# Optimization experiments

Measured on AMD Instinct MI355X. Metric: run time of the kernel, lower is better.

## Reference

```python
import jax, jax.numpy as jnp
import numpy as np

NUM_HEADS = 4
CATEGORY_SIZE = 128
DIM = 192
B, N, M = 2, 65000, 64


def setup_inputs() -> dict:
    key = jax.random.key(0)
    k1, k2, k3, k4 = jax.random.split(key, 4)
    qkv = jax.random.normal(k1, (B, N, 3 * DIM), dtype=jnp.float32)
    sim = jax.random.normal(k2, (B, N, M), dtype=jnp.float32)
    proj_w = jax.random.normal(k3, (DIM, DIM), dtype=jnp.float32) * (1.0 / np.sqrt(DIM))
    proj_b = jax.random.normal(k4, (DIM,), dtype=jnp.float32) * 0.01
    logit_scale = jnp.log(10.0 * jnp.ones((1, 1), dtype=jnp.float32))
    return {"qkv": qkv, "sim": sim, "proj_w": proj_w, "proj_b": proj_b,
            "logit_scale": logit_scale, "x_size": 65000}


def reference(qkv, sim, proj_w, proj_b, logit_scale, x_size):
    b, n, c3 = qkv.shape
    c = c3 // 3
    h = NUM_HEADS
    gs = min(n, CATEGORY_SIZE)
    ng = (n + gs - 1) // gs
    pad_n = ng * gs - n

    # token -> category id, then sort tokens by category
    tk_id = jnp.argmax(sim, axis=-1)                      # (b, n) int
    sort_idx = jnp.argsort(tk_id, axis=-1)                # (b, n)
    inv_idx = jnp.argsort(sort_idx, axis=-1)              # inverse permutation

    shuffled = jnp.take_along_axis(qkv, sort_idx[..., None], axis=1)  # (b, n, 3c)
    if pad_n > 0:
        pad = jnp.flip(shuffled[:, n - pad_n:n, :], axis=1)
        shuffled = jnp.concatenate([shuffled, pad], axis=1)           # (b, n+pad_n, 3c)

    # (3, b, ng, h, gs, c/h)
    y = shuffled.reshape(b, ng, gs, 3, h, c // h).transpose(3, 0, 1, 4, 2, 5)
    q, k, v = y[0], y[1], y[2]

    scale = jnp.exp(jnp.minimum(logit_scale, jnp.log(jnp.asarray(100.0, dtype=qkv.dtype))))
    attn = jnp.einsum('bghqd,bghkd->bghqk', q, k) * scale  # (b, ng, h, gs, gs)
    attn = jax.nn.softmax(attn, axis=-1)
    out = jnp.einsum('bghqk,bghkd->bghqd', attn, v)        # (b, ng, h, gs, c/h)
    out = out.transpose(0, 1, 3, 2, 4).reshape(b, n + pad_n, c)[:, :n, :]

    # scatter back to original token order
    out = jnp.take_along_axis(out, inv_idx[..., None], axis=1)
    return out @ proj_w.T + proj_b
```

## Files before the change

### kernel.cpp

```cpp
#include <hip/hip_runtime.h>
#include <hip/hip_bf16.h>
#include <math.h>

#define BB 2
#define NN 65000
#define MM 64
#define DIM 192
#define NH 4
#define HD 48
#define GS 128
#define NG 508
#define SORT_TPB 256
#define NBLK 254

#define XROWS 65024
#define XTILES_B 1016

typedef __attribute__((ext_vector_type(8))) short bf16x8;
typedef __attribute__((ext_vector_type(8))) _Float16 f16x8;
typedef __attribute__((ext_vector_type(2))) __fp16 fp16x2;
typedef __attribute__((ext_vector_type(4))) float f32x4;
typedef __attribute__((ext_vector_type(16))) float f32x16;
typedef __attribute__((ext_vector_type(8))) unsigned short u16x8;

__device__ __forceinline__ unsigned short f2bf(float f) {
  __hip_bfloat16 h = __float2bfloat16(f);
  return *(unsigned short*)&h;
}
__device__ __forceinline__ unsigned int pkh(float lo, float hi) {
  fp16x2 t = __builtin_amdgcn_cvt_pkrtz(lo, hi);
  return *(unsigned int*)&t;
}
__device__ __forceinline__ f16x8 cvt8h(float4 a, float4 b) {
  f16x8 r;
  r[0] = (_Float16)a.x; r[1] = (_Float16)a.y; r[2] = (_Float16)a.z; r[3] = (_Float16)a.w;
  r[4] = (_Float16)b.x; r[5] = (_Float16)b.y; r[6] = (_Float16)b.z; r[7] = (_Float16)b.w;
  return r;
}
__device__ __forceinline__ void gload_lds16(const float* src, float* lds_dst) {
  __builtin_amdgcn_global_load_lds(
      (const __attribute__((address_space(1))) unsigned int*)src,
      (__attribute__((address_space(3))) unsigned int*)lds_dst, 16, 0, 0);
}

__global__ void k_argmax_hist(const float* __restrict__ sim, int* __restrict__ tk,
                              int* __restrict__ hist) {
  __shared__ int cnt[MM];
  const int b = blockIdx.y, blk = blockIdx.x;
  if (threadIdx.x < MM) cnt[threadIdx.x] = 0;
  __syncthreads();
  int t = blk * SORT_TPB + threadIdx.x;
  if (t < NN) {
    const float4* row = (const float4*)(sim + ((size_t)b * NN + t) * MM);
    float best = -INFINITY;
    int bi = 0;
#pragma unroll
    for (int j = 0; j < MM / 4; ++j) {
      float4 v = row[j];
      if (v.x > best) { best = v.x; bi = 4 * j + 0; }
      if (v.y > best) { best = v.y; bi = 4 * j + 1; }
      if (v.z > best) { best = v.z; bi = 4 * j + 2; }
      if (v.w > best) { best = v.w; bi = 4 * j + 3; }
    }
    tk[b * NN + t] = bi;
    atomicAdd(&cnt[bi], 1);
  }
  __syncthreads();
  if (threadIdx.x < MM)
    hist[(b * NBLK + blk) * MM + threadIdx.x] = cnt[threadIdx.x];
}

#define SEGS 16
#define SEGB 16
__global__ void k_scan(const int* __restrict__ hist, int* __restrict__ boff) {
  const int b = blockIdx.x;
  const int tid = threadIdx.x;
  const int seg = tid >> 6, bin = tid & 63;
  __shared__ int part[SEGS][MM];
  __shared__ int basev[MM];
  const int lo = seg * SEGB;
  const int hi = min(NBLK, lo + SEGB);
  int s = 0;
  for (int blk = lo; blk < hi; ++blk) s += hist[(b * NBLK + blk) * MM + bin];
  part[seg][bin] = s;
  __syncthreads();
  if (tid < 64) {
    int tot = 0;
#pragma unroll
    for (int s2 = 0; s2 < SEGS; ++s2) tot += part[s2][bin];
    int incl = tot;
#pragma unroll
    for (int d = 1; d < 64; d <<= 1) {
      int o = __shfl_up(incl, d);
      if (bin >= d) incl += o;
    }
    basev[bin] = incl - tot;
  }
  __syncthreads();
  int run = basev[bin];
  for (int s2 = 0; s2 < seg; ++s2) run += part[s2][bin];
  for (int blk = lo; blk < hi; ++blk) {
    int h = hist[(b * NBLK + blk) * MM + bin];
    boff[(b * NBLK + blk) * MM + bin] = run;
    run += h;
  }
}

__global__ void k_scatter(const int* __restrict__ tk, const int* __restrict__ boff,
                          int* __restrict__ sidx) {
  __shared__ int whist[4][MM];
  const int b = blockIdx.y, blk = blockIdx.x;
  const int tid = threadIdx.x;
  const int w = tid >> 6, lane = tid & 63;
  ((int*)whist)[tid] = 0;
  __syncthreads();
  int t = blk * SORT_TPB + tid;
  int bin = (t < NN) ? tk[b * NN + t] : -1;
  unsigned long long m = ~0ull;
#pragma unroll
  for (int bit = 0; bit < 6; ++bit) {
    unsigned long long bl = __ballot((bin >> bit) & 1);
    m &= ((bin >> bit) & 1) ? bl : ~bl;
  }
  int rank_w = __popcll(m & ((1ull << lane) - 1ull));
  if (bin >= 0 && rank_w == 0) whist[w][bin] = __popcll(m);
  __syncthreads();
  if (bin >= 0) {
    int rank = rank_w;
#pragma unroll
    for (int w2 = 0; w2 < 3; ++w2)
      if (w2 < w) rank += whist[w2][bin];
    int pos = boff[(b * NBLK + blk) * MM + bin] + rank;
    sidx[b * NN + pos] = t;
  }
}

__global__ __launch_bounds__(256) void k_attn_mfma(const float* __restrict__ qkv,
                                                   const int* __restrict__ sidx,
                                                   const float* __restrict__ logit_scale,
                                                   __hip_bfloat16* __restrict__ attn_out) {
  const int x = blockIdx.x;
  const int g = ((x >> 4) << 3) + (x & 7);
  const int p = (x >> 3) & 1;
  const int b = blockIdx.z;
  if (g >= NG) return;
  const int hd0 = 2 * p;

  __shared__ int stok[GS];
  __shared__ __align__(16) _Float16 akv2[2][4 * 3 * 64 * 8];
  __shared__ __align__(16) _Float16 vfrag2[2][2 * 8 * 64 * 8];

  const int tid = threadIdx.x;
  const int w = tid >> 6, l = tid & 63;
  const int hl = l >> 5, l31 = l & 31;

  if (tid < GS) {
    int s = g * GS + tid;
    int sp = (s < NN) ? s : (2 * NN - 1 - s);
    stok[tid] = sidx[b * NN + sp];
  }
  __syncthreads();

#pragma unroll
  for (int head = 0; head < 2; ++head)
#pragma unroll
    for (int i = 0; i < 3; ++i) {
      int cc = tid + 256 * i;
      int ts = cc >> 6, cl = cc & 63;
      int kvr = (ts / 3) * 32 + (cl & 31);
      int dbase = (ts % 3) * 16 + (cl >> 5) * 8;
      const float* src = qkv + (size_t)(b * NN + stok[kvr]) * (3 * DIM) + DIM + (hd0 + head) * HD + dbase;
      ((f16x8*)akv2[head])[cc] = cvt8h(((const float4*)src)[0], ((const float4*)src)[1]);
    }

#pragma unroll
  for (int head = 0; head < 2; ++head)
#pragma unroll
    for (int i = 0; i < 4; ++i) {
      int cc = tid + 256 * i;
      int ntks = cc >> 6, cl = cc & 63;
      int nt = ntks >> 3, ks = ntks & 7;
      int d = nt * 32 + (cl & 31);
      int kvb = ks * 16 + (cl >> 5) * 8;
      _Float16 tmp[8];
      if (d < HD) {
#pragma unroll
        for (int e = 0; e < 8; ++e)
          tmp[e] = (_Float16)qkv[(size_t)(b * NN + stok[kvb + e]) * (3 * DIM) + 2 * DIM + (hd0 + head) * HD + d];
      } else {
#pragma unroll
        for (int e = 0; e < 8; ++e) tmp[e] = (_Float16)0.f;
      }
      ((f16x8*)vfrag2[head])[cc] = *(f16x8*)tmp;
    }

  f16x8 qf[2][3];
  {
    const float* qb = qkv + (size_t)(b * NN + stok[w * 32 + l31]) * (3 * DIM);
#pragma unroll
    for (int head = 0; head < 2; ++head)
#pragma unroll
      for (int s = 0; s < 3; ++s) {
        const float4* ptr = (const float4*)(qb + (hd0 + head) * HD + s * 16 + hl * 8);
        qf[head][s] = cvt8h(ptr[0], ptr[1]);
      }
  }
  __syncthreads();

  const float scale = expf(fminf(logit_scale[0], 4.6051701860f));

  for (int hh = 0; hh < 2; ++hh) {
    const int hd = hd0 + hh;

    f32x16 accS[4];
#pragma unroll
    for (int t = 0; t < 4; ++t)
#pragma unroll
      for (int r = 0; r < 16; ++r) accS[t][r] = 0.f;

#pragma unroll
    for (int t = 0; t < 4; ++t)
#pragma unroll
      for (int s = 0; s < 3; ++s) {
        f16x8 af = ((const f16x8*)akv2[hh])[(t * 3 + s) * 64 + l];
        accS[t] = __builtin_amdgcn_mfma_f32_32x32x16_f16(af, qf[hh][s], accS[t], 0, 0, 0);
      }

    float mx = -INFINITY;
#pragma unroll
    for (int t = 0; t < 4; ++t)
#pragma unroll
      for (int r = 0; r < 16; ++r) { accS[t][r] *= scale; mx = fmaxf(mx, accS[t][r]); }
    mx = fmaxf(mx, __shfl_xor(mx, 32));
    float sum = 0.f;
#pragma unroll
    for (int t = 0; t < 4; ++t)
#pragma unroll
      for (int r = 0; r < 16; ++r) { float pv = __expf(accS[t][r] - mx); accS[t][r] = pv; sum += pv; }
    sum += __shfl_xor(sum, 32);
    const float inv = 1.f / sum;
#pragma unroll
    for (int t = 0; t < 4; ++t)
#pragma unroll
      for (int r = 0; r < 16; ++r) accS[t][r] *= inv;

    f32x16 accO[2];
#pragma unroll
    for (int nt = 0; nt < 2; ++nt)
#pragma unroll
      for (int r = 0; r < 16; ++r) accO[nt][r] = 0.f;

#pragma unroll
    for (int t = 0; t < 4; ++t) {
      union { unsigned int u[4]; f16x8 v; } fa, fb;
      {
        unsigned int a0 = pkh(accS[t][0], accS[t][1]);
        unsigned int a1 = pkh(accS[t][2], accS[t][3]);
        unsigned int b0 = pkh(accS[t][4], accS[t][5]);
        unsigned int b1 = pkh(accS[t][6], accS[t][7]);
        unsigned int sa0 = __shfl_xor(a0, 32), sa1 = __shfl_xor(a1, 32);
        unsigned int sb0 = __shfl_xor(b0, 32), sb1 = __shfl_xor(b1, 32);
        fa.u[0] = hl ? sb0 : a0; fa.u[1] = hl ? sb1 : a1;
        fa.u[2] = hl ? b0 : sa0; fa.u[3] = hl ? b1 : sa1;
      }
      {
        unsigned int a0 = pkh(accS[t][8], accS[t][9]);
        unsigned int a1 = pkh(accS[t][10], accS[t][11]);
        unsigned int b0 = pkh(accS[t][12], accS[t][13]);
        unsigned int b1 = pkh(accS[t][14], accS[t][15]);
        unsigned int sa0 = __shfl_xor(a0, 32), sa1 = __shfl_xor(a1, 32);
        unsigned int sb0 = __shfl_xor(b0, 32), sb1 = __shfl_xor(b1, 32);
        fb.u[0] = hl ? sb0 : a0; fb.u[1] = hl ? sb1 : a1;
        fb.u[2] = hl ? b0 : sa0; fb.u[3] = hl ? b1 : sa1;
      }
      accO[0] = __builtin_amdgcn_mfma_f32_32x32x16_f16(fa.v, ((const f16x8*)vfrag2[hh])[(0 * 8 + 2 * t) * 64 + l], accO[0], 0, 0, 0);
      accO[1] = __builtin_amdgcn_mfma_f32_32x32x16_f16(fa.v, ((const f16x8*)vfrag2[hh])[(1 * 8 + 2 * t) * 64 + l], accO[1], 0, 0, 0);
      accO[0] = __builtin_amdgcn_mfma_f32_32x32x16_f16(fb.v, ((const f16x8*)vfrag2[hh])[(0 * 8 + 2 * t + 1) * 64 + l], accO[0], 0, 0, 0);
      accO[1] = __builtin_amdgcn_mfma_f32_32x32x16_f16(fb.v, ((const f16x8*)vfrag2[hh])[(1 * 8 + 2 * t + 1) * 64 + l], accO[1], 0, 0, 0);
    }

#pragma unroll
    for (int r = 0; r < 16; ++r) {
      int rowl = w * 32 + (r & 3) + 8 * (r >> 2) + 4 * hl;
      int sg = g * GS + rowl;
      if (sg < NN) {
        size_t base = ((size_t)b * XROWS + sg) * DIM + hd * HD;
        attn_out[base + l31] = __float2bfloat16(accO[0][r]);
        if (l31 < 16) attn_out[base + 32 + l31] = __float2bfloat16(accO[1][r]);
      }
    }
  }
}

__global__ void k_wpack(const float* __restrict__ W, unsigned short* __restrict__ wpack) {
  int idx = blockIdx.x * blockDim.x + threadIdx.x;
  if (idx >= 12 * 6 * 64) return;
  int lane = idx & 63;
  int kkjt = idx >> 6;
  int kk = kkjt % 6;
  int jt = kkjt / 6;
  int j = jt * 16 + (lane & 15);
  int k0 = kk * 32 + (lane >> 4) * 8;
  const float* src = W + (size_t)j * DIM + k0;
  unsigned short tmp[8];
#pragma unroll
  for (int e = 0; e < 8; ++e) tmp[e] = f2bf(src[e]);
  ((u16x8*)wpack)[idx] = *(const u16x8*)tmp;
}

__global__ __launch_bounds__(256) void k_proj_mfma(const unsigned short* __restrict__ xb,
                                                   const int* __restrict__ sidx,
                                                   const unsigned short* __restrict__ wpack,
                                                   const float* __restrict__ bias,
                                                   float* __restrict__ out) {
  __shared__ unsigned short wl[12 * 6 * 64 * 8];
  const int tid = threadIdx.x;

#pragma unroll
  for (int j = 0; j < 18; ++j) {
    int c = j * 256 + tid;
    gload_lds16((const float*)((const u16x8*)wpack + c), (float*)((u16x8*)wl + c));
  }

  const int wid = tid >> 6, lane = tid & 63;
  const int l15 = lane & 15, lk = lane >> 4;

  float bv[12];
#pragma unroll
  for (int jt = 0; jt < 12; ++jt) bv[jt] = bias[jt * 16 + l15];

  __syncthreads();

  for (int tile = blockIdx.x; tile < BB * XTILES_B; tile += gridDim.x) {
    const int b = tile / XTILES_B;
    const int r0 = (tile % XTILES_B) * 64 + wid * 16;
    f32x4 acc[12];
#pragma unroll
    for (int jt = 0; jt < 12; ++jt) { f32x4 t = {bv[jt], bv[jt], bv[jt], bv[jt]}; acc[jt] = t; }

    const unsigned short* xrow = xb + ((size_t)b * XROWS + r0 + l15) * DIM;
#pragma unroll
    for (int kk = 0; kk < 6; ++kk) {
      bf16x8 a = *(const bf16x8*)(xrow + kk * 32 + lk * 8);
#pragma unroll
      for (int jt = 0; jt < 12; ++jt) {
        bf16x8 bfr = *(const bf16x8*)(wl + ((jt * 6 + kk) * 64 + lane) * 8);
        acc[jt] = __builtin_amdgcn_mfma_f32_16x16x32_bf16(a, bfr, acc[jt], 0, 0, 0);
      }
    }

    const int rowb = r0 + lk * 4;
    int orow[4];
#pragma unroll
    for (int r = 0; r < 4; ++r)
      orow[r] = (rowb + r < NN) ? sidx[b * NN + rowb + r] : -1;

#pragma unroll
    for (int jt = 0; jt < 12; ++jt) {
#pragma unroll
      for (int r = 0; r < 4; ++r) {
        if (orow[r] >= 0)
          out[((size_t)b * NN + orow[r]) * DIM + jt * 16 + l15] = acc[jt][r];
      }
    }
  }
}

extern "C" void kernel_launch(void* const* d_in, const int* in_sizes, int n_in,
                              void* d_out, int out_size, void* d_ws, size_t ws_size,
                              hipStream_t stream) {
  const float* qkv = (const float*)d_in[0];
  const float* sim = (const float*)d_in[1];
  const float* proj_w = (const float*)d_in[2];
  const float* proj_b = (const float*)d_in[3];
  const float* logit_scale = (const float*)d_in[4];

  unsigned short* x_bf16 = (unsigned short*)d_ws;
  unsigned short* wpack = x_bf16 + (size_t)BB * XROWS * DIM;
  int* tk = (int*)(wpack + 12 * 6 * 64 * 8);
  int* hist = tk + (size_t)BB * NN;
  int* boff = hist + (size_t)BB * NBLK * MM;
  int* sidx = boff + (size_t)BB * NBLK * MM;

  k_argmax_hist<<<dim3(NBLK, BB), SORT_TPB, 0, stream>>>(sim, tk, hist);
  k_scan<<<BB, 1024, 0, stream>>>(hist, boff);
  k_scatter<<<dim3(NBLK, BB), SORT_TPB, 0, stream>>>(tk, boff, sidx);
  k_wpack<<<(12 * 6 * 64 + 255) / 256, 256, 0, stream>>>(proj_w, wpack);
  k_attn_mfma<<<dim3(1024, 1, BB), 256, 0, stream>>>(qkv, sidx, logit_scale,
                                                     (__hip_bfloat16*)x_bf16);
  k_proj_mfma<<<dim3(1016), 256, 0, stream>>>(x_bf16, sidx, wpack, proj_b, (float*)d_out);
}
```

Before: 171.0 us.

## Load K/V rows coalesced into padded LDS and gather MFMA fragments from LDS

Replaces the strided global gathers that built pre-swizzled K and V fragment buffers with coalesced float4 row loads of K and V into padded row-major LDS tiles (stride 100 halves). K fragments are then read from LDS as two 4-wide loads, and V fragments are built with scalar 16-bit LDS reads per element. The aim is to cut the scattered per-element global V loads; the cost is many more LDS instructions in the PV loop and possible bank conflicts. Launch bounds also now request 3 blocks per CU.

```diff
diff --git a/kernel.cpp b/kernel.cpp
--- a/kernel.cpp
+++ b/kernel.cpp
@@ -16,8 +16,11 @@
 #define XROWS 65024
 #define XTILES_B 1016
 
+#define KVS 100
+
 typedef __attribute__((ext_vector_type(8))) short bf16x8;
 typedef __attribute__((ext_vector_type(8))) _Float16 f16x8;
+typedef __attribute__((ext_vector_type(4))) _Float16 f16x4;
 typedef __attribute__((ext_vector_type(2))) __fp16 fp16x2;
 typedef __attribute__((ext_vector_type(4))) float f32x4;
 typedef __attribute__((ext_vector_type(16))) float f32x16;
@@ -135,20 +138,19 @@
   }
 }
 
-__global__ __launch_bounds__(256) void k_attn_mfma(const float* __restrict__ qkv,
-                                                   const int* __restrict__ sidx,
-                                                   const float* __restrict__ logit_scale,
-                                                   __hip_bfloat16* __restrict__ attn_out) {
+__global__ __launch_bounds__(256, 3) void k_attn_mfma(const float* __restrict__ qkv,
+                                                      const int* __restrict__ sidx,
+                                                      const float* __restrict__ logit_scale,
+                                                      __hip_bfloat16* __restrict__ attn_out) {
   const int x = blockIdx.x;
   const int g = ((x >> 4) << 3) + (x & 7);
   const int p = (x >> 3) & 1;
   const int b = blockIdx.z;
   if (g >= NG) return;
-  const int hd0 = 2 * p;
 
   __shared__ int stok[GS];
-  __shared__ __align__(16) _Float16 akv2[2][4 * 3 * 64 * 8];
-  __shared__ __align__(16) _Float16 vfrag2[2][2 * 8 * 64 * 8];
+  __shared__ __align__(16) _Float16 kls[GS * KVS];
+  __shared__ __align__(16) _Float16 vls[GS * KVS];
 
   const int tid = threadIdx.x;
   const int w = tid >> 6, l = tid & 63;
@@ -162,47 +164,28 @@
   __syncthreads();
 
 #pragma unroll
-  for (int head = 0; head < 2; ++head)
-#pragma unroll
-    for (int i = 0; i < 3; ++i) {
-      int cc = tid + 256 * i;
-      int ts = cc >> 6, cl = cc & 63;
-      int kvr = (ts / 3) * 32 + (cl & 31);
-      int dbase = (ts % 3) * 16 + (cl >> 5) * 8;
-      const float* src = qkv + (size_t)(b * NN + stok[kvr]) * (3 * DIM) + DIM + (hd0 + head) * HD + dbase;
-      ((f16x8*)akv2[head])[cc] = cvt8h(((const float4*)src)[0], ((const float4*)src)[1]);
-    }
-
-#pragma unroll
-  for (int head = 0; head < 2; ++head)
-#pragma unroll
-    for (int i = 0; i < 4; ++i) {
-      int cc = tid + 256 * i;
-      int ntks = cc >> 6, cl = cc & 63;
-      int nt = ntks >> 3, ks = ntks & 7;
-      int d = nt * 32 + (cl & 31);
-      int kvb = ks * 16 + (cl >> 5) * 8;
-      _Float16 tmp[8];
-      if (d < HD) {
-#pragma unroll
-        for (int e = 0; e < 8; ++e)
-          tmp[e] = (_Float16)qkv[(size_t)(b * NN + stok[kvb + e]) * (3 * DIM) + 2 * DIM + (hd0 + head) * HD + d];
-      } else {
-#pragma unroll
-        for (int e = 0; e < 8; ++e) tmp[e] = (_Float16)0.f;
-      }
-      ((f16x8*)vfrag2[head])[cc] = *(f16x8*)tmp;
-    }
+  for (int i = 0; i < 12; ++i) {
+    int c = tid + 256 * i;
+    int row = c / 24, piece = c % 24;
+    const float* base = qkv + (size_t)(b * NN + stok[row]) * (3 * DIM) + 96 * p + piece * 4;
+    float4 kv = *(const float4*)(base + DIM);
+    float4 vv = *(const float4*)(base + 2 * DIM);
+    f16x4 hk, hv;
+    hk[0] = (_Float16)kv.x; hk[1] = (_Float16)kv.y; hk[2] = (_Float16)kv.z; hk[3] = (_Float16)kv.w;
+    hv[0] = (_Float16)vv.x; hv[1] = (_Float16)vv.y; hv[2] = (_Float16)vv.z; hv[3] = (_Float16)vv.w;
+    *(f16x4*)(kls + row * KVS + piece * 4) = hk;
+    *(f16x4*)(vls + row * KVS + piece * 4) = hv;
+  }
 
   f16x8 qf[2][3];
   {
-    const float* qb = qkv + (size_t)(b * NN + stok[w * 32 + l31]) * (3 * DIM);
-#pragma unroll
-    for (int head = 0; head < 2; ++head)
+    const float* qsrc = qkv + (size_t)(b * NN + stok[w * 32 + l31]) * (3 * DIM) + 96 * p;
+#pragma unroll
+    for (int hh = 0; hh < 2; ++hh)
 #pragma unroll
       for (int s = 0; s < 3; ++s) {
-        const float4* ptr = (const float4*)(qb + (hd0 + head) * HD + s * 16 + hl * 8);
-        qf[head][s] = cvt8h(ptr[0], ptr[1]);
+        const float4* pp = (const float4*)(qsrc + hh * 48 + s * 16 + hl * 8);
+        qf[hh][s] = cvt8h(pp[0], pp[1]);
       }
   }
   __syncthreads();
@@ -210,7 +193,7 @@
   const float scale = expf(fminf(logit_scale[0], 4.6051701860f));
 
   for (int hh = 0; hh < 2; ++hh) {
-    const int hd = hd0 + hh;
+    const int hd = 2 * p + hh;
 
     f32x16 accS[4];
 #pragma unroll
@@ -222,7 +205,12 @@
     for (int t = 0; t < 4; ++t)
 #pragma unroll
       for (int s = 0; s < 3; ++s) {
-        f16x8 af = ((const f16x8*)akv2[hh])[(t * 3 + s) * 64 + l];
+        int kvr = t * 32 + l31;
+        const f16x4* ka = (const f16x4*)(kls + kvr * KVS + hh * 48 + s * 16 + hl * 8);
+        f16x4 a0 = ka[0], a1 = ka[1];
+        f16x8 af;
+        af[0] = a0[0]; af[1] = a0[1]; af[2] = a0[2]; af[3] = a0[3];
+        af[4] = a1[0]; af[5] = a1[1]; af[6] = a1[2]; af[7] = a1[3];
         accS[t] = __builtin_amdgcn_mfma_f32_32x32x16_f16(af, qf[hh][s], accS[t], 0, 0, 0);
       }
 
@@ -273,10 +261,28 @@
         fb.u[0] = hl ? sb0 : a0; fb.u[1] = hl ? sb1 : a1;
         fb.u[2] = hl ? b0 : sa0; fb.u[3] = hl ? b1 : sa1;
       }
-      accO[0] = __builtin_amdgcn_mfma_f32_32x32x16_f16(fa.v, ((const f16x8*)vfrag2[hh])[(0 * 8 + 2 * t) * 64 + l], accO[0], 0, 0, 0);
-      accO[1] = __builtin_amdgcn_mfma_f32_32x32x16_f16(fa.v, ((const f16x8*)vfrag2[hh])[(1 * 8 + 2 * t) * 64 + l], accO[1], 0, 0, 0);
-      accO[0] = __builtin_amdgcn_mfma_f32_32x32x16_f16(fb.v, ((const f16x8*)vfrag2[hh])[(0 * 8 + 2 * t + 1) * 64 + l], accO[0], 0, 0, 0);
-      accO[1] = __builtin_amdgcn_mfma_f32_32x32x16_f16(fb.v, ((const f16x8*)vfrag2[hh])[(1 * 8 + 2 * t + 1) * 64 + l], accO[1], 0, 0, 0);
+#pragma unroll
+      for (int j = 0; j < 2; ++j) {
+        const int ks = 2 * t + j;
+        const int r0 = ks * 16 + hl * 8;
+        f16x8 v0, v1;
+        {
+          const int d = l31;
+#pragma unroll
+          for (int e = 0; e < 8; ++e) v0[e] = vls[(r0 + e) * KVS + hh * 48 + d];
+        }
+        if (l31 < 16) {
+          const int d = 32 + l31;
+#pragma unroll
+          for (int e = 0; e < 8; ++e) v1[e] = vls[(r0 + e) * KVS + hh * 48 + d];
+        } else {
+#pragma unroll
+          for (int e = 0; e < 8; ++e) v1[e] = (_Float16)0.f;
+        }
+        const f16x8 pa = j ? fb.v : fa.v;
+        accO[0] = __builtin_amdgcn_mfma_f32_32x32x16_f16(pa, v0, accO[0], 0, 0, 0);
+        accO[1] = __builtin_amdgcn_mfma_f32_32x32x16_f16(pa, v1, accO[1], 0, 0, 0);
+      }
     }
 
 #pragma unroll
```

New measurement: 158.9 us (median of 2 runs). -7.1%, faster.
